# Performance work log

Hardware: AMD Instinct MI355X
Metric: run time of the kernel (lower is better)

Reference implementation:

```python
import jax, jax.numpy as jnp
import numpy as np

D_MODEL = 1024
N_HEADS = 16
D_HEAD = D_MODEL // N_HEADS


def setup_inputs() -> dict:
    key = jax.random.key(0)
    ks = jax.random.split(key, 16)
    B, S, D = 2, 2048, D_MODEL
    s = 1.0 / np.sqrt(D)
    inp = {
        "query": jax.random.normal(ks[0], (B, S, D), jnp.float32),
        "key": jax.random.normal(ks[1], (B, S, D), jnp.float32),
        "value": jax.random.normal(ks[2], (B, S, D), jnp.float32),
        "pos_embedding": jax.random.normal(ks[3], (B, S, D), jnp.float32),
        "Wq": jax.random.normal(ks[4], (D, D), jnp.float32) * s,
        "bq": jnp.zeros((D,), jnp.float32),
        "Wk": jax.random.normal(ks[5], (D, D), jnp.float32) * s,
        "bk": jnp.zeros((D,), jnp.float32),
        "Wv": jax.random.normal(ks[6], (D, D), jnp.float32) * s,
        "bv": jnp.zeros((D,), jnp.float32),
        "Wpos": jax.random.normal(ks[7], (D, D), jnp.float32) * s,
        "u_bias": jax.random.normal(ks[8], (N_HEADS, D_HEAD), jnp.float32) * s,
        "v_bias": jax.random.normal(ks[9], (N_HEADS, D_HEAD), jnp.float32) * s,
        "Wout": jax.random.normal(ks[10], (D, D), jnp.float32) * s,
        "bout": jnp.zeros((D,), jnp.float32),
    }
    return inp


def _rel_shift(pos_score):
    # Transformer-XL relative shift: pad one zero column, reshape, drop first row.
    B, H, S1, S2 = pos_score.shape
    zeros = jnp.zeros((B, H, S1, 1), pos_score.dtype)
    padded = jnp.concatenate([zeros, pos_score], axis=-1)  # [B,H,S1,S2+1]
    padded = padded.reshape(B, H, S2 + 1, S1)
    return padded[:, :, 1:].reshape(B, H, S1, S2)


def reference(query, key, value, pos_embedding, Wq, bq, Wk, bk, Wv, bv, Wpos, u_bias, v_bias, Wout, bout):
    B, S, D = query.shape
    H, dh = N_HEADS, D_HEAD
    q = (query @ Wq + bq).reshape(B, S, H, dh)            # [B,S,H,dh]
    k = (key @ Wk + bk).reshape(B, S, H, dh)              # [B,S,H,dh]
    v = (value @ Wv + bv).reshape(B, S, H, dh)            # [B,S,H,dh]
    p = (pos_embedding @ Wpos).reshape(B, S, H, dh)       # [B,S,H,dh]

    content_score = jnp.einsum('bqhd,bkhd->bhqk', q + u_bias, k)
    pos_score = jnp.einsum('bqhd,bkhd->bhqk', q + v_bias, p)
    pos_score = _rel_shift(pos_score)

    score = (content_score + pos_score) / jnp.asarray(np.sqrt(D), score_dtype := content_score.dtype)
    attn = jax.nn.softmax(score, axis=-1)                 # [B,H,S,S]
    context = jnp.einsum('bhqk,bkhd->bqhd', attn, v).reshape(B, S, D)
    out = context @ Wout + bout
    return out, attn
```

## Files before the change

### kernel.cpp

```cpp
#include <hip/hip_runtime.h>

#define S_LEN 2048
#define DM    1024
#define NH    16
#define DH    64
#define BATCH 2
#define S2    ((size_t)S_LEN * S_LEN)

typedef _Float16 half_t;
typedef _Float16 f16x8 __attribute__((ext_vector_type(8)));
typedef _Float16 f16x4 __attribute__((ext_vector_type(4)));
typedef float    f32x4 __attribute__((ext_vector_type(4)));

__device__ __forceinline__ void gll16(const void* g, void* l) {
  __builtin_amdgcn_global_load_lds(
      (const __attribute__((address_space(1))) void*)g,
      (__attribute__((address_space(3))) void*)l, 16, 0, 0);
}

__device__ __forceinline__ void stage_gll(half_t* lds, const half_t* src, int stride) {
  const int t = threadIdx.x, w = t >> 6, lane = t & 63;
  const int c1 = lane & 7, r8 = lane >> 3;
#pragma unroll
  for (int it = 0; it < 4; ++it) {
    int r = w * 32 + it * 8 + r8;
    const half_t* g = src + (size_t)r * stride + ((c1 ^ r8) << 3);
    gll16(g, lds + (size_t)w * 2048 + it * 512);
  }
}

__device__ __forceinline__ void mfma_block(const half_t* At, const half_t* Bt,
                                           int w, int lane, f32x4 acc[2][8]) {
  const int grp = lane >> 4, li = lane & 15;
#pragma unroll
  for (int ks = 0; ks < 2; ++ks) {
    const int chunk = ks * 4 + grp;
    f16x8 a[2], b[8];
#pragma unroll
    for (int fr = 0; fr < 2; ++fr) {
      int r = w * 32 + fr * 16 + li;
      a[fr] = *(const f16x8*)&At[(size_t)(r * 8 + (chunk ^ (r & 7))) * 8];
    }
#pragma unroll
    for (int fc = 0; fc < 8; ++fc) {
      int r = fc * 16 + li;
      b[fc] = *(const f16x8*)&Bt[(size_t)(r * 8 + (chunk ^ (r & 7))) * 8];
    }
#pragma unroll
    for (int fr = 0; fr < 2; ++fr)
#pragma unroll
      for (int fc = 0; fc < 8; ++fc)
        acc[fr][fc] = __builtin_amdgcn_mfma_f32_16x16x32_f16(a[fr], b[fc], acc[fr][fc], 0, 0, 0);
  }
}

template<typename ST>
__device__ __forceinline__ void load8s(const ST* p, float* o) {
  if constexpr (sizeof(ST) == 2) {
    f16x8 v = *(const f16x8*)p;
#pragma unroll
    for (int e = 0; e < 8; ++e) o[e] = (float)v[e];
  } else {
    const float4* q = (const float4*)p;
    float4 a = q[0], b = q[1];
    o[0]=a.x; o[1]=a.y; o[2]=a.z; o[3]=a.w; o[4]=b.x; o[5]=b.y; o[6]=b.z; o[7]=b.w;
  }
}

struct AArgs { const float* src[4]; half_t* dst[4]; };

__global__ __launch_bounds__(256) void a2h(AArgs a, half_t* zbuf) {
  if (blockIdx.x == 0 && blockIdx.y == 0 && threadIdx.x < 8) {
    float4 z = {0.f, 0.f, 0.f, 0.f};
    ((float4*)zbuf)[threadIdx.x] = z;
  }
  const float* s = a.src[blockIdx.y];
  half_t* d = a.dst[blockIdx.y];
  size_t i = ((size_t)blockIdx.x * 256 + threadIdx.x) * 8;
  float4 v0 = *(const float4*)(s + i), v1 = *(const float4*)(s + i + 4);
  f16x8 h;
  h[0]=(half_t)v0.x; h[1]=(half_t)v0.y; h[2]=(half_t)v0.z; h[3]=(half_t)v0.w;
  h[4]=(half_t)v1.x; h[5]=(half_t)v1.y; h[6]=(half_t)v1.z; h[7]=(half_t)v1.w;
  *(f16x8*)(d + i) = h;
}

struct WArgs { const float* src[5]; half_t* dst[5]; };

__global__ __launch_bounds__(256) void wconv(WArgs wa) {
  __shared__ float T[64][65];
  const float* W = wa.src[blockIdx.z];
  half_t* D = wa.dst[blockIdx.z];
  const int k0 = blockIdx.x * 64, n0 = blockIdx.y * 64;
  const int t = threadIdx.x;
#pragma unroll
  for (int it = 0; it < 4; ++it) {
    int idx = t + it * 256; int r = idx >> 4, c4 = (idx & 15) * 4;
    float4 v = *(const float4*)(W + (size_t)(k0 + r) * DM + n0 + c4);
    T[r][c4] = v.x; T[r][c4 + 1] = v.y; T[r][c4 + 2] = v.z; T[r][c4 + 3] = v.w;
  }
  __syncthreads();
#pragma unroll
  for (int it = 0; it < 2; ++it) {
    int idx = t + it * 256; int n = idx >> 3, kc = (idx & 7) * 8;
    f16x8 o;
#pragma unroll
    for (int e = 0; e < 8; ++e) o[e] = (half_t)T[kc + e][n];
    *(f16x8*)&D[(size_t)(n0 + n) * DM + k0 + kc] = o;
  }
}

struct GArgs {
  const half_t* A[4];  const half_t* Bt[4];
  const float* ba[4]; const float* bu[4]; const float* bv[4];
  half_t* oa[4]; half_t* ob[4]; float* of[4];
};

template<bool F32OUT>
__global__ __launch_bounds__(256) void gemm_k(GArgs g, int K) {
  __shared__ __align__(16) half_t At[128 * 64];
  __shared__ __align__(16) half_t Bt[128 * 64];
  const int z = blockIdx.z;
  const half_t* A = g.A[z];
  const half_t* B = g.Bt[z];
  const int n0 = blockIdx.x * 128, m0 = blockIdx.y * 128;
  const int t = threadIdx.x, w = t >> 6, lane = t & 63;
  const f32x4 zf = {0.f, 0.f, 0.f, 0.f};
  f32x4 acc[2][8];
#pragma unroll
  for (int i = 0; i < 2; ++i)
#pragma unroll
    for (int j = 0; j < 8; ++j) acc[i][j] = zf;

  for (int k0 = 0; k0 < K; k0 += 64) {
    stage_gll(At, A + (size_t)m0 * K + k0, K);
    stage_gll(Bt, B + (size_t)n0 * K + k0, K);
    __syncthreads();
    mfma_block(At, Bt, w, lane, acc);
    __syncthreads();
  }
  const int grp = lane >> 4, li = lane & 15;
#pragma unroll
  for (int fr = 0; fr < 2; ++fr)
#pragma unroll
    for (int fc = 0; fc < 8; ++fc)
#pragma unroll
      for (int r = 0; r < 4; ++r) {
        int row = m0 + w * 32 + fr * 16 + grp * 4 + r;
        int col = n0 + fc * 16 + li;
        float v = acc[fr][fc][r];
        if (g.ba[z]) v += g.ba[z][col];
        if constexpr (F32OUT) {
          g.of[z][(size_t)row * DM + col] = v;
        } else {
          float v1 = v + (g.bu[z] ? g.bu[z][col] : 0.f);
          g.oa[z][(size_t)row * DM + col] = (half_t)v1;
          if (g.ob[z]) g.ob[z][(size_t)row * DM + col] = (half_t)(v + g.bv[z][col]);
        }
      }
}

__global__ __launch_bounds__(256) void vtrans(const half_t* vp, half_t* vT) {
  __shared__ half_t T[64][72];
  const int s0 = blockIdx.x * 64, h = blockIdx.y, b = blockIdx.z;
  const int t = threadIdx.x;
#pragma unroll
  for (int it = 0; it < 2; ++it) {
    int idx = t + it * 256; int s = idx >> 3, c = idx & 7;
    uint4 v = *(const uint4*)(vp + ((size_t)(b * S_LEN + s0 + s)) * DM + h * DH + c * 8);
    *(uint4*)&T[s][c * 8] = v;
  }
  __syncthreads();
  half_t* dst = vT + ((size_t)(b * NH + h)) * DH * S_LEN;
#pragma unroll
  for (int it = 0; it < 2; ++it) {
    int idx = t + it * 256; int d = idx >> 3, sc = (idx & 7) * 8;
    f16x8 o;
#pragma unroll
    for (int e = 0; e < 8; ++e) o[e] = T[sc + e][d];
    *(f16x8*)&dst[(size_t)d * S_LEN + s0 + sc] = o;
  }
}

template<typename ST>
__global__ __launch_bounds__(512) void score_fused(
    const half_t* __restrict__ qu_, const half_t* __restrict__ qv_,
    const half_t* __restrict__ kp_, const half_t* __restrict__ pp_,
    const half_t* __restrict__ zbuf, ST* __restrict__ sc, float* __restrict__ part)
{
  __shared__ __align__(16) half_t Mf[36864];
  __shared__ __align__(16) half_t QV[144 * 64];
  __shared__ __align__(16) half_t Pb[256 * 64];
  half_t* QU = Mf;
  half_t* Kt = Mf + 8192;

  const int bh = blockIdx.z, b = bh >> 4, h = bh & 15;
  const int kt = blockIdx.x, qt = blockIdx.y;
  const int i0 = qt * 128, k0 = kt * 128;
  const int base = 1920 + k0 - i0;
  const int t = threadIdx.x, w = t >> 6, lane = t & 63;
  const int grp = lane >> 4, li = lane & 15;

  {
    const half_t* srcA = qu_ + ((size_t)(b * S_LEN + i0)) * DM + h * DH;
    const half_t* srcB = kp_ + ((size_t)(b * S_LEN + k0)) * DM + h * DH;
#pragma unroll
    for (int p = 0; p < 2; ++p) {
      int cidx = t + p * 512; int r = cidx >> 3, c = cidx & 7;
      gll16(srcA + (size_t)r * DM + ((c ^ (r & 7)) << 3), QU + (size_t)cidx * 8);
      gll16(srcB + (size_t)r * DM + ((c ^ (r & 7)) << 3), Kt + (size_t)cidx * 8);
    }
  }
#pragma unroll
  for (int p = 0; p < 3; ++p) {
    int cidx = t + p * 512;
    if (cidx < 1152) {
      int r = cidx >> 3, c = cidx & 7;
      int grow = i0 + r; if (grow > S_LEN - 1) grow = S_LEN - 1;
      gll16(qv_ + ((size_t)(b * S_LEN + grow)) * DM + h * DH + ((c ^ (r & 7)) << 3),
            QV + (size_t)cidx * 8);
    }
  }
#pragma unroll
  for (int p = 0; p < 4; ++p) {
    int cidx = t + p * 512; int e = cidx >> 3, c = cidx & 7;
    int jv = base + e; if (jv >= S_LEN + 1) jv -= (S_LEN + 1);
    const half_t* src = (jv == S_LEN)
        ? (zbuf + ((c ^ (e & 7)) << 3))
        : (pp_ + ((size_t)(b * S_LEN + jv)) * DM + h * DH + ((c ^ (e & 7)) << 3));
    gll16(src, Pb + (size_t)cidx * 8);
  }
  __syncthreads();

  const f32x4 zf = {0.f, 0.f, 0.f, 0.f};
  f32x4 acc_c[8];
#pragma unroll
  for (int j = 0; j < 8; ++j) acc_c[j] = zf;
#pragma unroll
  for (int kk = 0; kk < 2; ++kk) {
    const int chunk = kk * 4 + grp;
    int ra = w * 16 + li;
    f16x8 a = *(const f16x8*)&QU[(size_t)(ra * 8 + (chunk ^ (ra & 7))) * 8];
#pragma unroll
    for (int fc = 0; fc < 8; ++fc) {
      int rb = fc * 16 + li;
      f16x8 bf = *(const f16x8*)&Kt[(size_t)(rb * 8 + (chunk ^ (rb & 7))) * 8];
      acc_c[fc] = __builtin_amdgcn_mfma_f32_16x16x32_f16(a, bf, acc_c[fc], 0, 0, 0);
    }
  }
  __syncthreads();

  f16x8 bm[2][2];
#pragma unroll
  for (int kk = 0; kk < 2; ++kk)
#pragma unroll
    for (int eci = 0; eci < 2; ++eci) {
      int rb = (w + eci * 8) * 16 + li;
      bm[kk][eci] = *(const f16x8*)&Pb[(size_t)(rb * 8 + ((kk * 4 + grp) ^ (rb & 7))) * 8];
    }
  for (int rf = 0; rf < 9; ++rf) {
    f32x4 am[2] = {zf, zf};
#pragma unroll
    for (int kk = 0; kk < 2; ++kk) {
      int ra = rf * 16 + li;
      f16x8 a = *(const f16x8*)&QV[(size_t)(ra * 8 + ((kk * 4 + grp) ^ (ra & 7))) * 8];
#pragma unroll
      for (int eci = 0; eci < 2; ++eci)
        am[eci] = __builtin_amdgcn_mfma_f32_16x16x32_f16(a, bm[kk][eci], am[eci], 0, 0, 0);
    }
#pragma unroll
    for (int eci = 0; eci < 2; ++eci) {
      int ec = w + eci * 8;
      f16x4 hv;
#pragma unroll
      for (int r = 0; r < 4; ++r) hv[r] = (half_t)am[eci][r];
      *(f16x4*)&Mf[(size_t)(((ec * 9 + rf) * 4 + grp) * 64 + li * 4)] = hv;
    }
  }
  __syncthreads();

  ST* sb = sc + (size_t)bh * S2;
  float lsum[4] = {0.f, 0.f, 0.f, 0.f};
#pragma unroll
  for (int fc = 0; fc < 8; ++fc) {
#pragma unroll
    for (int rr = 0; rr < 4; ++rr) {
      int q = w * 16 + grp * 4 + rr;
      int k = fc * 16 + li;
      int e = k - q + 127;
      int jv = base + e;
      int dlt = (jv >= S_LEN + 1) ? 1 : 0;
      int rM = q + dlt;
      int ec = e >> 4, ei = e & 15, rf = rM >> 4, ri = rM & 15;
      float mval = (float)Mf[(size_t)(((ec * 9 + rf) * 4 + (ri >> 2)) * 64 + ei * 4 + (ri & 3))];
      float s = (acc_c[fc][rr] + mval) * 0.03125f;
      sb[(size_t)(i0 + q) * S_LEN + k0 + k] = (ST)s;
      lsum[rr] += __expf(s);
    }
  }
#pragma unroll
  for (int rr = 0; rr < 4; ++rr) {
    float v = lsum[rr];
#pragma unroll
    for (int d = 1; d < 16; d <<= 1) v += __shfl_xor(v, d);
    if (li == 0)
      part[((size_t)bh * S_LEN + i0 + w * 16 + grp * 4 + rr) * 16 + kt] = v;
  }
}

template<typename ST>
__global__ __launch_bounds__(256) void av_attn(const ST* sc, const half_t* vT, const float* part,
                                               float* attn, half_t* ctx) {
  __shared__ __align__(16) half_t Vt[64 * 128];
  __shared__ float Ls[128];
  const int bh = blockIdx.y, b = bh >> 4, h = bh & 15;
  const int q0 = blockIdx.x * 128;
  const int t = threadIdx.x;
  if (t < 128) {
    const float* pp = part + ((size_t)bh * S_LEN + q0 + t) * 16;
    float L = 0.f;
#pragma unroll
    for (int k = 0; k < 16; ++k) L += pp[k];
    Ls[t] = 1.f / L;
  }
  const ST* sb = sc + (size_t)bh * S2;
  float* ab = attn + (size_t)bh * S2;
  const half_t* vb = vT + (size_t)bh * (DH * S_LEN);
  const int w = t >> 6, lane = t & 63, grp = lane >> 4, li = lane & 15;
  const int c1 = lane & 15, d4 = lane >> 4;
  const f32x4 zf = {0.f, 0.f, 0.f, 0.f};
  f32x4 acc[2][4];
#pragma unroll
  for (int i = 0; i < 2; ++i)
#pragma unroll
    for (int j = 0; j < 4; ++j) acc[i][j] = zf;

  for (int kt = 0; kt < 16; ++kt) {
    __syncthreads();
#pragma unroll
    for (int it = 0; it < 4; ++it) {
      int d = w * 16 + it * 4 + d4;
      const half_t* g = vb + (size_t)d * S_LEN + kt * 128 + ((c1 ^ (d & 15)) << 3);
      gll16(g, Vt + (size_t)w * 2048 + it * 512);
    }
    __syncthreads();
#pragma unroll
    for (int ks = 0; ks < 4; ++ks) {
      f16x8 pa[2];
#pragma unroll
      for (int fr = 0; fr < 2; ++fr) {
        int r128 = w * 32 + fr * 16 + li;
        int row = q0 + r128;
        int col = kt * 128 + ks * 32 + grp * 8;
        float sv[8];
        load8s(&sb[(size_t)row * S_LEN + col], sv);
        float rL = Ls[r128];
#pragma unroll
        for (int e = 0; e < 8; ++e) sv[e] = __expf(sv[e]) * rL;
        float4* dst = (float4*)&ab[(size_t)row * S_LEN + col];
        float4 w0 = {sv[0], sv[1], sv[2], sv[3]};
        float4 w1 = {sv[4], sv[5], sv[6], sv[7]};
        dst[0] = w0; dst[1] = w1;
        f16x8 ph;
#pragma unroll
        for (int e = 0; e < 8; ++e) ph[e] = (half_t)sv[e];
        pa[fr] = ph;
      }
      f16x8 bf[4];
#pragma unroll
      for (int fc = 0; fc < 4; ++fc) {
        int d = fc * 16 + li; int chunk = ks * 4 + grp;
        bf[fc] = *(const f16x8*)&Vt[(size_t)(d * 16 + (chunk ^ (d & 15))) * 8];
      }
#pragma unroll
      for (int fr = 0; fr < 2; ++fr)
#pragma unroll
        for (int fc = 0; fc < 4; ++fc)
          acc[fr][fc] = __builtin_amdgcn_mfma_f32_16x16x32_f16(pa[fr], bf[fc], acc[fr][fc], 0, 0, 0);
    }
  }
#pragma unroll
  for (int fr = 0; fr < 2; ++fr)
#pragma unroll
    for (int fc = 0; fc < 4; ++fc)
#pragma unroll
      for (int r = 0; r < 4; ++r) {
        int q = q0 + w * 32 + fr * 16 + grp * 4 + r;
        int d = fc * 16 + li;
        ctx[((size_t)(b * S_LEN + q)) * DM + h * DH + d] = (half_t)acc[fr][fc][r];
      }
}

extern "C" void kernel_launch(void* const* d_in, const int* in_sizes, int n_in,
                              void* d_out, int out_size, void* d_ws, size_t ws_size,
                              hipStream_t stream) {
  (void)in_sizes; (void)n_in; (void)out_size;

  const float* query  = (const float*)d_in[0];
  const float* key    = (const float*)d_in[1];
  const float* value  = (const float*)d_in[2];
  const float* pos    = (const float*)d_in[3];
  const float* Wq     = (const float*)d_in[4];
  const float* bq     = (const float*)d_in[5];
  const float* Wk     = (const float*)d_in[6];
  const float* bk     = (const float*)d_in[7];
  const float* Wv     = (const float*)d_in[8];
  const float* bv     = (const float*)d_in[9];
  const float* Wpos   = (const float*)d_in[10];
  const float* u_bias = (const float*)d_in[11];
  const float* v_bias = (const float*)d_in[12];
  const float* Wout   = (const float*)d_in[13];
  const float* bout   = (const float*)d_in[14];

  float* out  = (float*)d_out;
  float* attn = out + (size_t)BATCH * S_LEN * DM;

  char* ws = (char*)d_ws;
  half_t* Wt   = (half_t*)(ws);
  half_t* Af16 = (half_t*)(ws + 10485760);
  float*  part = (float*)(ws + 10485760);
  half_t* qu   = (half_t*)(ws + 44040192);
  half_t* qv   = (half_t*)(ws + 52428800);
  half_t* kp   = (half_t*)(ws + 60817408);
  half_t* pp   = (half_t*)(ws + 69206016);
  half_t* vp   = (half_t*)(ws + 77594624);
  half_t* vT   = (half_t*)(ws + 85983232);
  half_t* ctx  = (half_t*)(ws + 77594624);
  half_t* zbuf = (half_t*)(ws + 94371840);
  half_t* scH  = (half_t*)(ws + 94375936);
  const bool fast = ws_size >= (size_t)94375936 + (size_t)BATCH * NH * S2 * 2;

  dim3 blk(256);

  AArgs aa;
  aa.src[0] = query; aa.src[1] = key; aa.src[2] = value; aa.src[3] = pos;
  for (int i = 0; i < 4; ++i) aa.dst[i] = Af16 + (size_t)i * BATCH * S_LEN * DM;
  a2h<<<dim3(2048, 4), blk, 0, stream>>>(aa, zbuf);

  WArgs wa;
  wa.src[0] = Wq; wa.src[1] = Wk; wa.src[2] = Wv; wa.src[3] = Wpos; wa.src[4] = Wout;
  for (int i = 0; i < 5; ++i) wa.dst[i] = Wt + (size_t)i * DM * DM;
  wconv<<<dim3(16, 16, 5), blk, 0, stream>>>(wa);

  GArgs ga{};
  for (int i = 0; i < 4; ++i) {
    ga.A[i]  = Af16 + (size_t)i * BATCH * S_LEN * DM;
    ga.Bt[i] = Wt + (size_t)i * DM * DM;
  }
  ga.ba[0] = bq; ga.ba[1] = bk; ga.ba[2] = bv; ga.ba[3] = nullptr;
  ga.bu[0] = u_bias; ga.bv[0] = v_bias;
  ga.oa[0] = qu; ga.oa[1] = kp; ga.oa[2] = vp; ga.oa[3] = pp;
  ga.ob[0] = qv;
  gemm_k<false><<<dim3(8, 32, 4), blk, 0, stream>>>(ga, DM);

  vtrans<<<dim3(32, 16, 2), blk, 0, stream>>>(vp, vT);

  dim3 g_sc(16, 16, 32);
  dim3 blk5(512);
  if (fast) {
    score_fused<half_t><<<g_sc, blk5, 0, stream>>>(qu, qv, kp, pp, zbuf, scH, part);
    av_attn<half_t><<<dim3(16, 32), blk, 0, stream>>>(scH, vT, part, attn, ctx);
  } else {
    float* scF = attn;
    score_fused<float><<<g_sc, blk5, 0, stream>>>(qu, qv, kp, pp, zbuf, scF, part);
    av_attn<float><<<dim3(16, 32), blk, 0, stream>>>(scF, vT, part, attn, ctx);
  }

  GArgs go{};
  go.A[0] = ctx; go.Bt[0] = Wt + (size_t)4 * DM * DM;
  go.ba[0] = bout; go.of[0] = out;
  gemm_k<true><<<dim3(8, 32, 1), blk, 0, stream>>>(go, DM);
}
```

Measured before the change: 597.8 us.

## Double-buffer LDS staging in GEMM and AV kernels; store exp scores

Both the projection GEMM and the attention-times-V kernel now use two LDS buffers, issuing the async global-to-LDS loads for the next K tile before running MFMAs on the current one. This overlaps memory latency with compute and cuts one barrier per iteration. The score kernel now stores exp(score) instead of the raw score, so the AV kernel only multiplies by the reciprocal row sum and no longer recomputes the exponential. Doubling LDS per block may lower occupancy. Storing exp values without max subtraction in the half-precision path risks overflow if scores are large.

```diff
diff --git a/kernel.cpp b/kernel.cpp
--- a/kernel.cpp
+++ b/kernel.cpp
@@ -117,8 +117,8 @@
 
 template<bool F32OUT>
 __global__ __launch_bounds__(256) void gemm_k(GArgs g, int K) {
-  __shared__ __align__(16) half_t At[128 * 64];
-  __shared__ __align__(16) half_t Bt[128 * 64];
+  __shared__ __align__(16) half_t At[2][128 * 64];
+  __shared__ __align__(16) half_t Bt[2][128 * 64];
   const int z = blockIdx.z;
   const half_t* A = g.A[z];
   const half_t* B = g.Bt[z];
@@ -131,12 +131,19 @@
 #pragma unroll
     for (int j = 0; j < 8; ++j) acc[i][j] = zf;
 
+  stage_gll(At[0], A + (size_t)m0 * K, K);
+  stage_gll(Bt[0], B + (size_t)n0 * K, K);
+  __syncthreads();
+  int cur = 0;
   for (int k0 = 0; k0 < K; k0 += 64) {
-    stage_gll(At, A + (size_t)m0 * K + k0, K);
-    stage_gll(Bt, B + (size_t)n0 * K + k0, K);
+    int nk = k0 + 64;
+    if (nk < K) {
+      stage_gll(At[cur ^ 1], A + (size_t)m0 * K + nk, K);
+      stage_gll(Bt[cur ^ 1], B + (size_t)n0 * K + nk, K);
+    }
+    mfma_block(At[cur], Bt[cur], w, lane, acc);
     __syncthreads();
-    mfma_block(At, Bt, w, lane, acc);
-    __syncthreads();
+    cur ^= 1;
   }
   const int grp = lane >> 4, li = lane & 15;
 #pragma unroll
@@ -293,8 +300,9 @@
       int ec = e >> 4, ei = e & 15, rf = rM >> 4, ri = rM & 15;
       float mval = (float)Mf[(size_t)(((ec * 9 + rf) * 4 + (ri >> 2)) * 64 + ei * 4 + (ri & 3))];
       float s = (acc_c[fc][rr] + mval) * 0.03125f;
-      sb[(size_t)(i0 + q) * S_LEN + k0 + k] = (ST)s;
-      lsum[rr] += __expf(s);
+      float ev = __expf(s);
+      sb[(size_t)(i0 + q) * S_LEN + k0 + k] = (ST)ev;
+      lsum[rr] += ev;
     }
   }
 #pragma unroll
@@ -310,7 +318,7 @@
 template<typename ST>
 __global__ __launch_bounds__(256) void av_attn(const ST* sc, const half_t* vT, const float* part,
                                                float* attn, half_t* ctx) {
-  __shared__ __align__(16) half_t Vt[64 * 128];
+  __shared__ __align__(16) half_t Vt[2][64 * 128];
   __shared__ float Ls[128];
   const int bh = blockIdx.y, b = bh >> 4, h = bh & 15;
   const int q0 = blockIdx.x * 128;
@@ -334,15 +342,23 @@
 #pragma unroll
     for (int j = 0; j < 4; ++j) acc[i][j] = zf;
 
+#pragma unroll
+  for (int it = 0; it < 4; ++it) {
+    int d = w * 16 + it * 4 + d4;
+    gll16(vb + (size_t)d * S_LEN + ((c1 ^ (d & 15)) << 3), Vt[0] + (size_t)w * 2048 + it * 512);
+  }
+  __syncthreads();
+  int cur = 0;
+
   for (int kt = 0; kt < 16; ++kt) {
-    __syncthreads();
-#pragma unroll
-    for (int it = 0; it < 4; ++it) {
-      int d = w * 16 + it * 4 + d4;
-      const half_t* g = vb + (size_t)d * S_LEN + kt * 128 + ((c1 ^ (d & 15)) << 3);
-      gll16(g, Vt + (size_t)w * 2048 + it * 512);
-    }
-    __syncthreads();
+    if (kt + 1 < 16) {
+#pragma unroll
+      for (int it = 0; it < 4; ++it) {
+        int d = w * 16 + it * 4 + d4;
+        gll16(vb + (size_t)d * S_LEN + (kt + 1) * 128 + ((c1 ^ (d & 15)) << 3),
+              Vt[cur ^ 1] + (size_t)w * 2048 + it * 512);
+      }
+    }
 #pragma unroll
     for (int ks = 0; ks < 4; ++ks) {
       f16x8 pa[2];
@@ -355,7 +371,7 @@
         load8s(&sb[(size_t)row * S_LEN + col], sv);
         float rL = Ls[r128];
 #pragma unroll
-        for (int e = 0; e < 8; ++e) sv[e] = __expf(sv[e]) * rL;
+        for (int e = 0; e < 8; ++e) sv[e] *= rL;
         float4* dst = (float4*)&ab[(size_t)row * S_LEN + col];
         float4 w0 = {sv[0], sv[1], sv[2], sv[3]};
         float4 w1 = {sv[4], sv[5], sv[6], sv[7]};
@@ -369,7 +385,7 @@
 #pragma unroll
       for (int fc = 0; fc < 4; ++fc) {
         int d = fc * 16 + li; int chunk = ks * 4 + grp;
-        bf[fc] = *(const f16x8*)&Vt[(size_t)(d * 16 + (chunk ^ (d & 15))) * 8];
+        bf[fc] = *(const f16x8*)&Vt[cur][(size_t)(d * 16 + (chunk ^ (d & 15))) * 8];
       }
 #pragma unroll
       for (int fr = 0; fr < 2; ++fr)
@@ -377,6 +393,8 @@
         for (int fc = 0; fc < 4; ++fc)
           acc[fr][fc] = __builtin_amdgcn_mfma_f32_16x16x32_f16(pa[fr], bf[fc], acc[fr][fc], 0, 0, 0);
     }
+    __syncthreads();
+    cur ^= 1;
   }
 #pragma unroll
   for (int fr = 0; fr < 2; ++fr)
@@ -408,8 +426,8 @@
   const float* Wpos   = (const float*)d_in[10];
   const float* u_bias = (const float*)d_in[11];
   const float* v_bias = (const float*)d_in[12];
+  const float* bout   = (const float*)d_in[14];
   const float* Wout   = (const float*)d_in[13];
-  const float* bout   = (const float*)d_in[14];
 
   float* out  = (float*)d_out;
   float* attn = out + (size_t)BATCH * S_LEN * DM;
```

After: 585.8 us. 2.0% less time.
